# Optimization experiments

Measured on AMD Instinct MI355X. Metric: run time of the kernel, lower is better.

Reference implementation:

```python
import jax, jax.numpy as jnp
import numpy as np

N_NODES = 50000
N_EDGES = 800000
D1 = 64
D2 = 32
N_CLASSES = 6
N_LAYERS = 2
N_GRAPHS = 128


def setup_inputs() -> dict:
    key = jax.random.key(0)
    ks = jax.random.split(key, 12)
    x = jax.random.normal(ks[0], (N_NODES, D1), dtype=jnp.float32)
    edge_index = jax.random.randint(ks[1], (2, N_EDGES), 0, N_NODES, dtype=jnp.int32)
    batch_vector = jnp.sort(jax.random.randint(ks[2], (N_NODES,), 0, N_GRAPHS, dtype=jnp.int32))
    s = 1.0 / np.sqrt(D1)
    W = jax.random.uniform(ks[3], (N_LAYERS, D1, D1), jnp.float32, -s, s)
    w_ih = jax.random.uniform(ks[4], (3 * D1, D1), jnp.float32, -s, s)
    w_hh = jax.random.uniform(ks[5], (3 * D1, D1), jnp.float32, -s, s)
    b_ih = jax.random.uniform(ks[6], (3 * D1,), jnp.float32, -s, s)
    b_hh = jax.random.uniform(ks[7], (3 * D1,), jnp.float32, -s, s)
    fc1_w = jax.random.uniform(ks[8], (D2, D1), jnp.float32, -s, s)
    fc1_b = jnp.zeros((D2,), jnp.float32)
    fc2_w = jax.random.uniform(ks[9], (N_CLASSES, D2), jnp.float32, -1.0 / np.sqrt(D2), 1.0 / np.sqrt(D2))
    fc2_b = jnp.zeros((N_CLASSES,), jnp.float32)
    return {"x": x, "edge_index": edge_index, "batch_vector": batch_vector,
            "W": W, "w_ih": w_ih, "w_hh": w_hh, "b_ih": b_ih, "b_hh": b_hh,
            "fc1_w": fc1_w, "fc1_b": fc1_b, "fc2_w": fc2_w, "fc2_b": fc2_b}


def _gru_cell(m, h, w_ih, w_hh, b_ih, b_hh):
    # PyTorch GRUCell semantics
    gi = m @ w_ih.T + b_ih            # [N, 3D]
    gh = h @ w_hh.T + b_hh            # [N, 3D]
    i_r, i_z, i_n = jnp.split(gi, 3, axis=1)
    h_r, h_z, h_n = jnp.split(gh, 3, axis=1)
    r = jax.nn.sigmoid(i_r + h_r)
    z = jax.nn.sigmoid(i_z + h_z)
    n = jnp.tanh(i_n + r * h_n)
    return (1.0 - z) * n + z * h


def reference(x, edge_index, batch_vector, W, w_ih, w_hh, b_ih, b_hh,
              fc1_w, fc1_b, fc2_w, fc2_b):
    src, dst = edge_index[0], edge_index[1]
    h = x  # feature dim == out_channels, no padding needed
    for i in range(N_LAYERS):
        m = h @ W[i]                                   # [N, D1]
        msg = m[src]                                   # gather per-edge [E, D1]
        agg = jax.ops.segment_sum(msg, dst, num_segments=N_NODES)  # scatter-add
        h = _gru_cell(agg, h, w_ih, w_hh, b_ih, b_hh)
    h = jax.nn.relu(h)
    # dropout is identity in eval mode
    # global mean pool over graphs
    sums = jax.ops.segment_sum(h, batch_vector, num_segments=N_GRAPHS)
    counts = jax.ops.segment_sum(jnp.ones((N_NODES,), h.dtype), batch_vector, num_segments=N_GRAPHS)
    pooled = sums / jnp.maximum(counts, 1.0)[:, None]   # [G, D1]
    out = jax.nn.relu(pooled @ fc1_w.T + fc1_b)
    out = out @ fc2_w.T + fc2_b
    return jax.nn.log_softmax(out, axis=1)
```

## Files before the change

### kernel.cpp

```cpp
#include <hip/hip_runtime.h>

#define N_NODES 50000
#define N_EDGES 800000
#define D1 64
#define D2 32
#define N_CLASSES 6
#define N_GRAPHS 128
#define CAP 64
#define GB 782
#define GRUT 3125

#define NBINS 196
#define BCAP 6144
#define EPB 4096
#define NFILLB 196
#define LCAP 48
#define FH_BLOCKS (NFILLB + GB + 128 + 16 + 1)

typedef unsigned short u16;
typedef unsigned int u32;
typedef __attribute__((ext_vector_type(4))) int i32x4;
typedef __attribute__((ext_vector_type(4))) unsigned int u32x4;
typedef __attribute__((ext_vector_type(8))) short bf16x8;
typedef __attribute__((ext_vector_type(4))) float f32x4;

__device__ __forceinline__ float bf2f(u16 b) {
    u32 u = ((u32)b) << 16;
    float f;
    __builtin_memcpy(&f, &u, 4);
    return f;
}
__device__ __forceinline__ u16 f2bf(float f) {
    u32 u;
    __builtin_memcpy(&u, &f, 4);
    u32 r = (u + 0x7fffu + ((u >> 16) & 1u)) >> 16;
    return (u16)r;
}
__device__ __forceinline__ void split8(const float* v, bf16x8& hi, bf16x8& lo) {
#pragma unroll
    for (int j = 0; j < 8; ++j) {
        u16 h = f2bf(v[j]);
        hi[j] = (short)h;
        lo[j] = (short)f2bf(v[j] - bf2f(h));
    }
}
__device__ __forceinline__ void round8(const float* v, bf16x8& b) {
#pragma unroll
    for (int j = 0; j < 8; ++j) b[j] = (short)f2bf(v[j]);
}
__device__ __forceinline__ float sigmoidf_(float x) {
    return 1.0f / (1.0f + __expf(-x));
}
__device__ __forceinline__ float tanhf_(float x) {
    return 1.0f - 2.0f / (__expf(2.0f * x) + 1.0f);
}

__global__ __launch_bounds__(256) void fused_head_kernel(
        const int* __restrict__ ei, u32* __restrict__ binned, u32* __restrict__ binCursor,
        const float* __restrict__ x, const float* __restrict__ W,
        const float* __restrict__ wih, const float* __restrict__ whh,
        const float* __restrict__ bih, const float* __restrict__ bhh,
        short* __restrict__ Bh, short* __restrict__ Wp, float* __restrict__ bias4,
        u16* __restrict__ m16) {
    __shared__ u32 cnt[NBINS];
    __shared__ u32 base[NBINS];
    __shared__ u32 buck[NBINS][LCAP];
    int b = blockIdx.x;
    int tid = threadIdx.x;
    if (b < NFILLB) {
        for (int i = tid; i < NBINS; i += 256) cnt[i] = 0;
        __syncthreads();
        int e0 = b * EPB;
        int nq = (min(EPB, N_EDGES - e0)) >> 2;
        const i32x4* s4 = (const i32x4*)ei + (e0 >> 2);
        const i32x4* d4 = (const i32x4*)(ei + N_EDGES) + (e0 >> 2);
#pragma unroll
        for (int ch = 0; ch < 4; ++ch) {
            int i = ch * 256 + tid;
            if (i < nq) {
                i32x4 ss = s4[i];
                i32x4 dd = d4[i];
#pragma unroll
                for (int j = 0; j < 4; ++j) {
                    int s = ss[j];
                    int d = dd[j];
                    int bin = d >> 8;
                    u32 pay = ((u32)s << 8) | (u32)(d & 255);
                    u32 p = atomicAdd(&cnt[bin], 1u);
                    if (p < LCAP) buck[bin][p] = pay;
                    else {
                        u32 q = atomicAdd(&binCursor[bin], 1u);
                        if (q < BCAP) binned[bin * BCAP + q] = pay;
                    }
                }
            }
        }
        __syncthreads();
        int lane = tid & 63, wv = tid >> 6;
        if (lane < 49) {
            int bin = wv * 49 + lane;
            u32 c = cnt[bin];
            c = c < (u32)LCAP ? c : (u32)LCAP;
            base[bin] = atomicAdd(&binCursor[bin], c);
        }
        __syncthreads();
        for (int idx = 0; idx < 49; ++idx) {
            int bin = wv * 49 + idx;
            u32 c = cnt[bin];
            c = c < (u32)LCAP ? c : (u32)LCAP;
            if ((u32)lane < c) {
                u32 pos = base[bin] + lane;
                if (pos < BCAP) binned[bin * BCAP + pos] = buck[bin][lane];
            }
        }
        return;
    }
    int ob = b - NFILLB;
    if (ob < GB) {
        int lane = tid & 63;
        int wv = tid >> 6;
        int node0 = ob * 64 + wv * 16;
        if (node0 >= N_NODES) return;
        int c0 = lane & 15, qr = lane >> 4;
        f32x4 acc[4];
#pragma unroll
        for (int nt = 0; nt < 4; ++nt) acc[nt] = (f32x4){0.f, 0.f, 0.f, 0.f};
#pragma unroll
        for (int kt = 0; kt < 2; ++kt) {
            int aoff = (node0 + c0) * 64 + kt * 32 + qr * 8;
            float tmp[8];
#pragma unroll
            for (int j = 0; j < 8; ++j) tmp[j] = x[aoff + j];
            int k0 = kt * 32 + qr * 8;
            float wt[4][8];
#pragma unroll
            for (int nt = 0; nt < 4; ++nt)
#pragma unroll
                for (int j = 0; j < 8; ++j) wt[nt][j] = W[(k0 + j) * 64 + nt * 16 + c0];
            bf16x8 ah, al;
            split8(tmp, ah, al);
#pragma unroll
            for (int nt = 0; nt < 4; ++nt) {
                bf16x8 bb;
                round8(wt[nt], bb);
                acc[nt] = __builtin_amdgcn_mfma_f32_16x16x32_bf16(ah, bb, acc[nt], 0, 0, 0);
                acc[nt] = __builtin_amdgcn_mfma_f32_16x16x32_bf16(al, bb, acc[nt], 0, 0, 0);
            }
        }
#pragma unroll
        for (int nt = 0; nt < 4; ++nt)
#pragma unroll
            for (int r = 0; r < 4; ++r)
                m16[(node0 + qr * 4 + r) * 64 + nt * 16 + c0] = f2bf(acc[nt][r]);
    } else if (ob < GB + 128) {
        int idx = (ob - GB) * 256 + tid;
        int j = idx & 7;
        int lane = (idx >> 3) & 63;
        int nt = (idx >> 9) & 15;
        int step = idx >> 13;
        int k = step * 32 + (lane >> 4) * 8 + j;
        int n = nt * 16 + (lane & 15);
        int g = n >> 6, d = n & 63;
        float v;
        if (g == 0)      v = (k < 64) ? wih[d * 64 + k] : whh[d * 64 + (k - 64)];
        else if (g == 1) v = (k < 64) ? wih[(64 + d) * 64 + k] : whh[(64 + d) * 64 + (k - 64)];
        else if (g == 2) v = (k < 64) ? wih[(128 + d) * 64 + k] : 0.f;
        else             v = (k < 64) ? 0.f : whh[(128 + d) * 64 + (k - 64)];
        Bh[idx] = (short)f2bf(v);
    } else if (ob < GB + 144) {
        int idx2 = (ob - (GB + 128)) * 256 + tid;
        int j = idx2 & 7;
        int lane = (idx2 >> 3) & 63;
        int nt = (idx2 >> 9) & 3;
        int kt = idx2 >> 11;
        Wp[idx2] = (short)f2bf(
            W[4096 + (kt * 32 + (lane >> 4) * 8 + j) * 64 + nt * 16 + (lane & 15)]);
    } else {
        int j = tid;
        if (j < 64) {
            bias4[j] = bih[j] + bhh[j];
            bias4[64 + j] = bih[64 + j] + bhh[64 + j];
            bias4[128 + j] = bih[128 + j];
            bias4[192 + j] = bhh[128 + j];
        }
    }
}

__global__ __launch_bounds__(256) void bucket_kernel(
        const u32* __restrict__ binned, const u32* __restrict__ binCursor,
        int* __restrict__ deg, u16* __restrict__ srcidx) {
    __shared__ u32 ndeg[256];
    __shared__ __align__(16) u16 nb[256][CAP];
    int bin = blockIdx.x;
    int tid = threadIdx.x;
    ndeg[tid] = 0;
    __syncthreads();
    int c = (int)binCursor[bin];
    if (c > BCAP) c = BCAP;
    const u32* src = binned + bin * BCAP;
    for (int i = tid; i < c; i += 256) {
        u32 pay = src[i];
        int dl = pay & 255;
        u32 p = atomicAdd(&ndeg[dl], 1u);
        if (p < CAP) nb[dl][p] = (u16)(pay >> 8);
    }
    __syncthreads();
    int node0 = bin * 256;
    int nn = N_NODES - node0;
    if (nn > 256) nn = 256;
    u32x4* dst16 = (u32x4*)(srcidx + (size_t)node0 * CAP);
    const u32x4* src16 = (const u32x4*)nb;
    int tot = nn * 8;
    for (int i = tid; i < tot; i += 256) dst16[i] = src16[i];
    if (tid < nn) {
        u32 d = ndeg[tid];
        deg[node0 + tid] = (int)(d < (u32)CAP ? d : (u32)CAP);
    }
}

__global__ __launch_bounds__(256) void agg_kernel(const u16* __restrict__ m16,
                                                  const int* __restrict__ deg,
                                                  const u16* __restrict__ srcidx,
                                                  float* __restrict__ aggf) {
    int lane = threadIdx.x & 63;
    int node = blockIdx.x * 4 + (threadIdx.x >> 6);
    int cnt = __builtin_amdgcn_readfirstlane(deg[node]);
    cnt = cnt < CAP ? cnt : CAP;
    int bv = (int)srcidx[node * CAP + lane];
    int half = lane >> 5;
    int l = lane & 31;
    const u32* m32 = (const u32*)m16;
    float a0 = 0.f, a1 = 0.f;
    int k = half;
    for (; k + 6 < cnt; k += 8) {
        int s0 = __shfl(bv, k);
        int s1 = __shfl(bv, k + 2);
        int s2 = __shfl(bv, k + 4);
        int s3 = __shfl(bv, k + 6);
        u32 d0 = m32[s0 * 32 + l];
        u32 d1 = m32[s1 * 32 + l];
        u32 d2 = m32[s2 * 32 + l];
        u32 d3 = m32[s3 * 32 + l];
        a0 += bf2f((u16)d0) + bf2f((u16)d1) + bf2f((u16)d2) + bf2f((u16)d3);
        a1 += bf2f((u16)(d0 >> 16)) + bf2f((u16)(d1 >> 16)) +
              bf2f((u16)(d2 >> 16)) + bf2f((u16)(d3 >> 16));
    }
    for (; k < cnt; k += 2) {
        int s = __shfl(bv, k);
        u32 d = m32[s * 32 + l];
        a0 += bf2f((u16)d);
        a1 += bf2f((u16)(d >> 16));
    }
    a0 += __shfl_xor(a0, 32);
    a1 += __shfl_xor(a1, 32);
    if (half == 0) {
        float2 st;
        st.x = a0;
        st.y = a1;
        ((float2*)aggf)[node * 32 + l] = st;
    }
}

template <bool DO_MM>
__global__ __launch_bounds__(256) void gru_kernel(
        const float* __restrict__ aggf, const short* __restrict__ Bh,
        const short* __restrict__ Wp, const float* __restrict__ bias4,
        const float* hin,
        float* hout, u16* __restrict__ m16) {
    __shared__ __align__(16) float tiles[DO_MM ? 4 * 16 * 65 : 4];
    int tid = threadIdx.x;
    int lane = tid & 63;
    int wv = tid >> 6;
    int wtask = blockIdx.x * 4 + wv;
    if (wtask >= GRUT) return;
    int node0 = wtask * 16;
    int c = lane & 15, q = lane >> 4;
    int rowA = node0 + c;
    float* myTile = tiles + (DO_MM ? wv * 16 * 65 : 0);

    f32x4 acc[16];
#pragma unroll
    for (int nt = 0; nt < 16; ++nt) acc[nt] = (f32x4){0.f, 0.f, 0.f, 0.f};

#pragma unroll
    for (int step = 0; step < 4; ++step) {
        const float* src = (step < 2) ? aggf : hin;
        int aoff = rowA * 64 + (step & 1) * 32 + q * 8;
        float tmp[8];
#pragma unroll
        for (int j = 0; j < 8; ++j) tmp[j] = src[aoff + j];
        bf16x8 bfr[8];
#pragma unroll
        for (int nt = 0; nt < 8; ++nt)
            bfr[nt] = *(const bf16x8*)(Bh + (step * 16 + nt) * 512 + lane * 8);
        bf16x8 ah, al;
        split8(tmp, ah, al);
#pragma unroll
        for (int nt = 0; nt < 8; ++nt) {
            acc[nt] = __builtin_amdgcn_mfma_f32_16x16x32_bf16(ah, bfr[nt], acc[nt], 0, 0, 0);
            acc[nt] = __builtin_amdgcn_mfma_f32_16x16x32_bf16(al, bfr[nt], acc[nt], 0, 0, 0);
        }
        bf16x8 bfr2[8];
#pragma unroll
        for (int nt = 0; nt < 8; ++nt)
            bfr2[nt] = *(const bf16x8*)(Bh + (step * 16 + 8 + nt) * 512 + lane * 8);
#pragma unroll
        for (int nt = 0; nt < 8; ++nt) {
            acc[8 + nt] =
                __builtin_amdgcn_mfma_f32_16x16x32_bf16(ah, bfr2[nt], acc[8 + nt], 0, 0, 0);
            acc[8 + nt] =
                __builtin_amdgcn_mfma_f32_16x16x32_bf16(al, bfr2[nt], acc[8 + nt], 0, 0, 0);
        }
    }

#pragma unroll
    for (int reg = 0; reg < 4; ++reg) {
        int R = q * 4 + reg;
        int row = node0 + R;
#pragma unroll
        for (int jt = 0; jt < 4; ++jt) {
            int j = jt * 16 + c;
            float rr = sigmoidf_(acc[jt][reg] + bias4[j]);
            float zz = sigmoidf_(acc[4 + jt][reg] + bias4[64 + j]);
            float nn = tanhf_(acc[8 + jt][reg] + bias4[128 + j] +
                              rr * (acc[12 + jt][reg] + bias4[192 + j]));
            float ho = hin[row * 64 + j];
            float v = (1.f - zz) * nn + zz * ho;
            hout[row * 64 + j] = v;
            if (DO_MM) myTile[R * 65 + j] = v;
        }
    }

    if (DO_MM) {
        f32x4 macc[4];
#pragma unroll
        for (int nt = 0; nt < 4; ++nt) macc[nt] = (f32x4){0.f, 0.f, 0.f, 0.f};
#pragma unroll
        for (int kt = 0; kt < 2; ++kt) {
            int k0 = kt * 32 + q * 8;
            bf16x8 wf[4];
#pragma unroll
            for (int nt = 0; nt < 4; ++nt)
                wf[nt] = *(const bf16x8*)(Wp + ((kt * 4 + nt) * 64 + lane) * 8);
            float tmp[8];
#pragma unroll
            for (int j = 0; j < 8; ++j) tmp[j] = myTile[c * 65 + k0 + j];
            bf16x8 aa;
            round8(tmp, aa);
#pragma unroll
            for (int nt = 0; nt < 4; ++nt)
                macc[nt] = __builtin_amdgcn_mfma_f32_16x16x32_bf16(aa, wf[nt], macc[nt], 0, 0, 0);
        }
#pragma unroll
        for (int nt = 0; nt < 4; ++nt)
#pragma unroll
            for (int reg = 0; reg < 4; ++reg)
                m16[(node0 + q * 4 + reg) * 64 + nt * 16 + c] = f2bf(macc[nt][reg]);
    }
}

__global__ __launch_bounds__(256) void poolhead_kernel(const float* __restrict__ h,
                                                       const int* __restrict__ batch,
                                                       const float* __restrict__ fc1w,
                                                       const float* __restrict__ fc1b,
                                                       const float* __restrict__ fc2w,
                                                       const float* __restrict__ fc2b,
                                                       float* __restrict__ out) {
    int g = blockIdx.x;
    int tid = threadIdx.x, lane = tid & 63, wv = tid >> 6;
    int lo, hi;
    {
        int a = 0, b = N_NODES;
        while (a < b) { int mid = (a + b) >> 1; if (batch[mid] < g) a = mid + 1; else b = mid; }
        lo = a;
    }
    {
        int a = lo, b = N_NODES;
        while (a < b) { int mid = (a + b) >> 1; if (batch[mid] < g + 1) a = mid + 1; else b = mid; }
        hi = a;
    }
    float acc = 0.f;
    for (int n = lo + wv; n < hi; n += 4) acc += fmaxf(h[n * 64 + lane], 0.f);
    __shared__ float red[4][64];
    __shared__ float pv[64];
    __shared__ float s1[32];
    __shared__ float s2[6];
    red[wv][lane] = acc;
    __syncthreads();
    if (tid < 64)
        pv[tid] = (red[0][tid] + red[1][tid] + red[2][tid] + red[3][tid]) /
                  fmaxf((float)(hi - lo), 1.f);
    __syncthreads();
    if (tid < 32) {
        float a2 = fc1b[tid];
#pragma unroll
        for (int j = 0; j < 64; ++j) a2 = fmaf(pv[j], fc1w[tid * 64 + j], a2);
        s1[tid] = fmaxf(a2, 0.f);
    }
    __syncthreads();
    if (tid < 6) {
        float a2 = fc2b[tid];
#pragma unroll
        for (int j = 0; j < 32; ++j) a2 = fmaf(s1[j], fc2w[tid * 32 + j], a2);
        s2[tid] = a2;
    }
    __syncthreads();
    if (tid == 0) {
        float mx = s2[0];
#pragma unroll
        for (int c = 1; c < 6; ++c) mx = fmaxf(mx, s2[c]);
        float se = 0.f;
#pragma unroll
        for (int c = 0; c < 6; ++c) se += __expf(s2[c] - mx);
        float lse = mx + __logf(se);
#pragma unroll
        for (int c = 0; c < 6; ++c) out[g * 6 + c] = s2[c] - lse;
    }
}

extern "C" void kernel_launch(void* const* d_in, const int* in_sizes, int n_in,
                              void* d_out, int out_size, void* d_ws, size_t ws_size,
                              hipStream_t stream) {
    const float* x    = (const float*)d_in[0];
    const int* ei     = (const int*)d_in[1];
    const int* batch  = (const int*)d_in[2];
    const float* W    = (const float*)d_in[3];
    const float* wih  = (const float*)d_in[4];
    const float* whh  = (const float*)d_in[5];
    const float* bih  = (const float*)d_in[6];
    const float* bhh  = (const float*)d_in[7];
    const float* fc1w = (const float*)d_in[8];
    const float* fc1b = (const float*)d_in[9];
    const float* fc2w = (const float*)d_in[10];
    const float* fc2b = (const float*)d_in[11];
    float* out = (float*)d_out;

    float* h       = (float*)d_ws;
    float* bias4   = h + N_NODES * D1;
    int* deg       = (int*)(bias4 + 256);
    u16* srcidx    = (u16*)(deg + N_NODES);
    size_t soff = ((size_t)(srcidx + N_NODES * CAP) + 15) & ~(size_t)15;
    u16* m16    = (u16*)soff;
    float* aggf = (float*)(m16 + N_NODES * D1);
    short* Bh   = (short*)(aggf + N_NODES * D1);
    short* Wp   = Bh + 32768;
    u32* binCursor = (u32*)(Wp + 4096);
    u32* binned = (u32*)aggf;

    hipMemsetAsync(binCursor, 0, NBINS * sizeof(u32), stream);
    fused_head_kernel<<<FH_BLOCKS, 256, 0, stream>>>(
        ei, binned, binCursor, x, W, wih, whh, bih, bhh, Bh, Wp, bias4, m16);
    bucket_kernel<<<NBINS, 256, 0, stream>>>(binned, binCursor, deg, srcidx);

    agg_kernel<<<N_NODES / 4, 256, 0, stream>>>(m16, deg, srcidx, aggf);
    gru_kernel<true><<<GB, 256, 0, stream>>>(aggf, Bh, Wp, bias4, x, h, m16);
    agg_kernel<<<N_NODES / 4, 256, 0, stream>>>(m16, deg, srcidx, aggf);
    gru_kernel<false><<<GB, 256, 0, stream>>>(aggf, Bh, Wp, bias4, h, h, nullptr);

    poolhead_kernel<<<N_GRAPHS, 256, 0, stream>>>(h, batch, fc1w, fc1b, fc2w, fc2b, out);
}
```

Measured before the change: 237.5 us.

## Fuse ReLU and mean-pool sums into final GRU kernel via atomics

The last GRU layer no longer writes h to memory. It applies ReLU and accumulates per-graph sums into a zeroed gsum buffer, reducing within each 16-node wave tile through shuffles when all nodes share a graph and falling back to per-element atomics otherwise. The pooling kernel shrinks to a 64-thread head that only divides by counts and runs the MLP and log-softmax. Input rows are also preloaded into registers before the MFMA loop. This removes a full write and reread of the 50000x64 float h, at the cost of atomic contention on the 128 graph rows and float summation order that is no longer deterministic.

```diff
diff --git a/kernel.cpp b/kernel.cpp
--- a/kernel.cpp
+++ b/kernel.cpp
@@ -266,7 +266,8 @@
         const float* __restrict__ aggf, const short* __restrict__ Bh,
         const short* __restrict__ Wp, const float* __restrict__ bias4,
         const float* hin,
-        float* hout, u16* __restrict__ m16) {
+        float* hout, u16* __restrict__ m16,
+        const int* __restrict__ batch, float* __restrict__ gsum) {
     __shared__ __align__(16) float tiles[DO_MM ? 4 * 16 * 65 : 4];
     int tid = threadIdx.x;
     int lane = tid & 63;
@@ -278,17 +279,25 @@
     int rowA = node0 + c;
     float* myTile = tiles + (DO_MM ? wv * 16 * 65 : 0);
 
+    const float* aggrow = aggf + rowA * 64 + q * 8;
+    const float* hinrow = hin + rowA * 64 + q * 8;
+    float av0[8], av1[8], hv0[8], hv1[8];
+#pragma unroll
+    for (int j = 0; j < 8; ++j) av0[j] = aggrow[j];
+#pragma unroll
+    for (int j = 0; j < 8; ++j) av1[j] = aggrow[32 + j];
+#pragma unroll
+    for (int j = 0; j < 8; ++j) hv0[j] = hinrow[j];
+#pragma unroll
+    for (int j = 0; j < 8; ++j) hv1[j] = hinrow[32 + j];
+
     f32x4 acc[16];
 #pragma unroll
     for (int nt = 0; nt < 16; ++nt) acc[nt] = (f32x4){0.f, 0.f, 0.f, 0.f};
 
 #pragma unroll
     for (int step = 0; step < 4; ++step) {
-        const float* src = (step < 2) ? aggf : hin;
-        int aoff = rowA * 64 + (step & 1) * 32 + q * 8;
-        float tmp[8];
-#pragma unroll
-        for (int j = 0; j < 8; ++j) tmp[j] = src[aoff + j];
+        const float* tmp = (step == 0) ? av0 : (step == 1) ? av1 : (step == 2) ? hv0 : hv1;
         bf16x8 bfr[8];
 #pragma unroll
         for (int nt = 0; nt < 8; ++nt)
@@ -313,6 +322,13 @@
         }
     }
 
+    float psum[4] = {0.f, 0.f, 0.f, 0.f};
+    int b0 = 0;
+    bool uniform = false;
+    if (!DO_MM) {
+        b0 = batch[node0];
+        uniform = (b0 == batch[node0 + 15]);
+    }
 #pragma unroll
     for (int reg = 0; reg < 4; ++reg) {
         int R = q * 4 + reg;
@@ -326,9 +342,28 @@
                               rr * (acc[12 + jt][reg] + bias4[192 + j]));
             float ho = hin[row * 64 + j];
             float v = (1.f - zz) * nn + zz * ho;
-            hout[row * 64 + j] = v;
-            if (DO_MM) myTile[R * 65 + j] = v;
-        }
+            if (DO_MM) {
+                hout[row * 64 + j] = v;
+                myTile[R * 65 + j] = v;
+            } else {
+                float rv = fmaxf(v, 0.f);
+                if (uniform) psum[jt] += rv;
+                else atomicAdd(&gsum[batch[row] * 64 + j], rv);
+            }
+        }
+    }
+
+    if (!DO_MM) {
+        if (uniform) {
+#pragma unroll
+            for (int jt = 0; jt < 4; ++jt) {
+                psum[jt] += __shfl_xor(psum[jt], 16);
+                psum[jt] += __shfl_xor(psum[jt], 32);
+            }
+            float emit = q == 0 ? psum[0] : q == 1 ? psum[1] : q == 2 ? psum[2] : psum[3];
+            atomicAdd(&gsum[b0 * 64 + q * 16 + c], emit);
+        }
+        return;
     }
 
     if (DO_MM) {
@@ -359,15 +394,15 @@
     }
 }
 
-__global__ __launch_bounds__(256) void poolhead_kernel(const float* __restrict__ h,
-                                                       const int* __restrict__ batch,
-                                                       const float* __restrict__ fc1w,
-                                                       const float* __restrict__ fc1b,
-                                                       const float* __restrict__ fc2w,
-                                                       const float* __restrict__ fc2b,
-                                                       float* __restrict__ out) {
+__global__ __launch_bounds__(64) void head_kernel(const float* __restrict__ gsum,
+                                                  const int* __restrict__ batch,
+                                                  const float* __restrict__ fc1w,
+                                                  const float* __restrict__ fc1b,
+                                                  const float* __restrict__ fc2w,
+                                                  const float* __restrict__ fc2b,
+                                                  float* __restrict__ out) {
     int g = blockIdx.x;
-    int tid = threadIdx.x, lane = tid & 63, wv = tid >> 6;
+    int tid = threadIdx.x;
     int lo, hi;
     {
         int a = 0, b = N_NODES;
@@ -379,17 +414,10 @@
         while (a < b) { int mid = (a + b) >> 1; if (batch[mid] < g + 1) a = mid + 1; else b = mid; }
         hi = a;
     }
-    float acc = 0.f;
-    for (int n = lo + wv; n < hi; n += 4) acc += fmaxf(h[n * 64 + lane], 0.f);
-    __shared__ float red[4][64];
     __shared__ float pv[64];
     __shared__ float s1[32];
     __shared__ float s2[6];
-    red[wv][lane] = acc;
-    __syncthreads();
-    if (tid < 64)
-        pv[tid] = (red[0][tid] + red[1][tid] + red[2][tid] + red[3][tid]) /
-                  fmaxf((float)(hi - lo), 1.f);
+    pv[tid] = gsum[g * 64 + tid] / fmaxf((float)(hi - lo), 1.f);
     __syncthreads();
     if (tid < 32) {
         float a2 = fc1b[tid];
@@ -445,17 +473,19 @@
     short* Bh   = (short*)(aggf + N_NODES * D1);
     short* Wp   = Bh + 32768;
     u32* binCursor = (u32*)(Wp + 4096);
+    float* gsum = (float*)(binCursor + NBINS);
     u32* binned = (u32*)aggf;
 
-    hipMemsetAsync(binCursor, 0, NBINS * sizeof(u32), stream);
+    hipMemsetAsync(binCursor, 0, NBINS * sizeof(u32) + N_GRAPHS * D1 * sizeof(float), stream);
     fused_head_kernel<<<FH_BLOCKS, 256, 0, stream>>>(
         ei, binned, binCursor, x, W, wih, whh, bih, bhh, Bh, Wp, bias4, m16);
     bucket_kernel<<<NBINS, 256, 0, stream>>>(binned, binCursor, deg, srcidx);
 
     agg_kernel<<<N_NODES / 4, 256, 0, stream>>>(m16, deg, srcidx, aggf);
-    gru_kernel<true><<<GB, 256, 0, stream>>>(aggf, Bh, Wp, bias4, x, h, m16);
+    gru_kernel<true><<<GB, 256, 0, stream>>>(aggf, Bh, Wp, bias4, x, h, m16, batch, gsum);
     agg_kernel<<<N_NODES / 4, 256, 0, stream>>>(m16, deg, srcidx, aggf);
-    gru_kernel<false><<<GB, 256, 0, stream>>>(aggf, Bh, Wp, bias4, h, h, nullptr);
-
-    poolhead_kernel<<<N_GRAPHS, 256, 0, stream>>>(h, batch, fc1w, fc1b, fc2w, fc2b, out);
-}
+    gru_kernel<false><<<GB, 256, 0, stream>>>(aggf, Bh, Wp, bias4, h, nullptr, nullptr,
+                                              batch, gsum);
+
+    head_kernel<<<N_GRAPHS, 64, 0, stream>>>(gsum, batch, fc1w, fc1b, fc2w, fc2b, out);
+}
```

New measurement: 223.6 us. 5.9% less time.
